# Optimization experiments

Hardware: AMD Instinct MI355X
Metric: run time of the kernel (lower is better)

The kernel has to match this reference:

```python
import jax, jax.numpy as jnp
import numpy as np

B, T, D, H = 16, 2048, 1024, 1024  # batch, seq (effective block_size), n_embed, head_size


def setup_inputs() -> dict:
    key = jax.random.key(0)
    k1, k2, k3, k4 = jax.random.split(key, 4)
    x = jax.random.normal(k1, (B, T, D), dtype=jnp.float32)
    # torch Linear weight is [out,in]; store as [in,out] for x @ W
    s = 1.0 / np.sqrt(D)
    Wq = jax.random.uniform(k2, (D, H), dtype=jnp.float32, minval=-s, maxval=s)
    Wk = jax.random.uniform(k3, (D, H), dtype=jnp.float32, minval=-s, maxval=s)
    Wv = jax.random.uniform(k4, (D, H), dtype=jnp.float32, minval=-s, maxval=s)
    return {"x": x, "Wq": Wq, "Wk": Wk, "Wv": Wv}


def reference(x, Wq, Wk, Wv):
    # Single-head causal self-attention, NO 1/sqrt(d) scaling (faithful to source).
    q = x @ Wq  # [B,T,H]
    k = x @ Wk  # [B,T,H]
    v = x @ Wv  # [B,T,H]
    w = jnp.einsum('bth,bsh->bts', q, k)  # [B,T,T]
    Tn = x.shape[1]
    causal = jnp.tril(jnp.ones((Tn, Tn), dtype=bool))
    w = jnp.where(causal, w, -jnp.inf)
    w = jax.nn.softmax(w, axis=-1)
    # dropout is identity in eval mode
    out = jnp.einsum('bts,bsh->bth', w, v)  # [B,T,H]
    return out
```

## Files before the change

### kernel.cpp

```cpp
#include <hip/hip_runtime.h>
#include <hip/hip_bf16.h>


typedef _Float16 half8 __attribute__((ext_vector_type(8)));
typedef _Float16 half4v __attribute__((ext_vector_type(4)));
typedef float floatx4 __attribute__((ext_vector_type(4)));

#define TB 16
#define TT 2048
#define TD 1024

__global__ void cvt_f32_f16(const float* __restrict__ in, _Float16* __restrict__ out, long n) {
    long i = ((long)blockIdx.x * blockDim.x + threadIdx.x) * 4;
    long stride = (long)gridDim.x * blockDim.x * 4;
    for (; i < n; i += stride) {
        float4 f = *(const float4*)(in + i);
        half4v h;
        h[0] = (_Float16)f.x; h[1] = (_Float16)f.y;
        h[2] = (_Float16)f.z; h[3] = (_Float16)f.w;
        *(half4v*)(out + i) = h;
    }
}

__global__ void transpose_cvt_w(const float* __restrict__ in, _Float16* __restrict__ out) {
    __shared__ float tile[32][33];
    const int bx = blockIdx.x * 32, by = blockIdx.y * 32;
    const int tx = threadIdx.x, ty = threadIdx.y;
#pragma unroll
    for (int i = ty; i < 32; i += 8) tile[i][tx] = in[(long)(by + i) * 1024 + bx + tx];
    __syncthreads();
#pragma unroll
    for (int i = ty; i < 32; i += 8) out[(long)(bx + i) * 1024 + by + tx] = (_Float16)tile[tx][i];
}

__device__ __forceinline__ void gload16(const _Float16* g, _Float16* l) {
    __builtin_amdgcn_global_load_lds((const __attribute__((address_space(1))) void*)g,
                                     (__attribute__((address_space(3))) void*)l, 16, 0, 0);
}

template <int MODE>
__global__ __launch_bounds__(512, 2) void gemm256(const _Float16* __restrict__ A,
                                                  const _Float16* __restrict__ B,
                                                  void* __restrict__ Cout,
                                                  int K, int lda, int ldb, int ldc,
                                                  long sAb, long sBb, long sCb,
                                                  int tilesN, int tilesM) {
    __shared__ _Float16 lds[65536];
    const int tid = threadIdx.x, lane = tid & 63, w = tid >> 6;
    const int wr = w >> 2, wc = w & 3;

    int bx = blockIdx.x;
    {
        const int nwg = gridDim.x, q = nwg >> 3, r = nwg & 7;
        const int xcd = bx & 7, idx = bx >> 3;
        bx = (xcd < r ? xcd * (q + 1) : r * (q + 1) + (xcd - r) * q) + idx;
    }
    int ti, tj;
    if (MODE == 1) {
        int rd = bx; ti = 0;
        while (rd > ti) { rd -= ti + 1; ++ti; }
        tj = rd;
    } else {
        ti = bx / tilesN; tj = bx % tilesN;
        if (MODE == 2) ti = tilesM - 1 - ti;
    }
    const int b = blockIdx.y;
    A += (long)b * sAb;
    B += (long)b * sBb;
    const long m0 = (long)ti * 256, n0 = (long)tj * 256;
    const int nkt = (MODE == 2) ? (ti + 1) * 4 : (K >> 6);

    const int row0 = tid >> 2;
    const int co   = (((tid & 3) ^ ((tid >> 3) & 3)) << 3);
    const int fcol = ((((lane >> 4) ^ (lane >> 1)) & 3) << 3);
    const int arow = wr * 128 + (lane & 15);
    const int brow = wc * 64 + (lane & 15);

    auto Abase = [&](int buf, int kk) { return lds + ((buf * 2 + kk) << 13); };
    auto Bbase = [&](int buf, int kk) { return lds + 32768 + ((buf * 2 + kk) << 13); };

    auto stageA = [&](int buf, int kk, int kt) {
        const long kb = (long)kt * 64 + kk * 32 + co;
        _Float16* d = Abase(buf, kk) + (w << 9);
        gload16(A + (m0 + row0) * (long)lda + kb, d);
        gload16(A + (m0 + row0 + 128) * (long)lda + kb, d + 4096);
    };
    auto stageB = [&](int buf, int kk, int kt) {
        const long kb = (long)kt * 64 + kk * 32 + co;
        _Float16* d = Bbase(buf, kk) + (w << 9);
        gload16(B + (n0 + row0) * (long)ldb + kb, d);
        gload16(B + (n0 + row0 + 128) * (long)ldb + kb, d + 4096);
    };
    auto ldA = [&](int buf, int kk, int m) {
        return *(const half8*)(Abase(buf, kk) + (arow + m * 16) * 32 + fcol);
    };
    auto ldB = [&](int buf, int kk, int n) {
        return *(const half8*)(Bbase(buf, kk) + (brow + n * 16) * 32 + fcol);
    };

    floatx4 acc[8][4] = {};

#define MFMA16(MH)                                                                     \
    _Pragma("unroll") for (int mm = 0; mm < 4; ++mm)                                   \
    _Pragma("unroll") for (int nn = 0; nn < 4; ++nn)                                   \
        acc[(MH)*4 + mm][nn] =                                                         \
            __builtin_amdgcn_mfma_f32_16x16x32_f16(afr[mm], bfr[nn], acc[(MH)*4 + mm][nn], 0, 0, 0);

    stageA(0, 0, 0); stageB(0, 0, 0); stageA(0, 1, 0); stageB(0, 1, 0);
    asm volatile("s_waitcnt vmcnt(4)" ::: "memory");
    __builtin_amdgcn_s_barrier();

    for (int t = 0; t < nkt; ++t) {
        const int cur = t & 1, nxt = cur ^ 1;
        const bool pf = (t + 1 < nkt);
        const int kn = t + 1;
        half8 afr[4], bfr[4];
#pragma unroll
        for (int nn = 0; nn < 4; ++nn) bfr[nn] = ldB(cur, 0, nn);
#pragma unroll
        for (int mm = 0; mm < 4; ++mm) afr[mm] = ldA(cur, 0, mm);
        if (pf) stageA(nxt, 0, kn);
        __builtin_amdgcn_s_barrier();
        asm volatile("s_waitcnt lgkmcnt(0)" ::: "memory");
        __builtin_amdgcn_sched_barrier(0);
        __builtin_amdgcn_s_setprio(1);
        MFMA16(0)
        __builtin_amdgcn_s_setprio(0);
        __builtin_amdgcn_s_barrier();
#pragma unroll
        for (int mm = 0; mm < 4; ++mm) afr[mm] = ldA(cur, 0, mm + 4);
        if (pf) stageB(nxt, 0, kn);
        __builtin_amdgcn_s_barrier();
        asm volatile("s_waitcnt lgkmcnt(0)" ::: "memory");
        __builtin_amdgcn_sched_barrier(0);
        __builtin_amdgcn_s_setprio(1);
        MFMA16(1)
        __builtin_amdgcn_s_setprio(0);
        if (pf) { asm volatile("s_waitcnt vmcnt(4)" ::: "memory"); }
        else    { asm volatile("s_waitcnt vmcnt(0)" ::: "memory"); }
        __builtin_amdgcn_s_barrier();
#pragma unroll
        for (int nn = 0; nn < 4; ++nn) bfr[nn] = ldB(cur, 1, nn);
#pragma unroll
        for (int mm = 0; mm < 4; ++mm) afr[mm] = ldA(cur, 1, mm);
        if (pf) stageA(nxt, 1, kn);
        __builtin_amdgcn_s_barrier();
        asm volatile("s_waitcnt lgkmcnt(0)" ::: "memory");
        __builtin_amdgcn_sched_barrier(0);
        __builtin_amdgcn_s_setprio(1);
        MFMA16(0)
        __builtin_amdgcn_s_setprio(0);
        __builtin_amdgcn_s_barrier();
#pragma unroll
        for (int mm = 0; mm < 4; ++mm) afr[mm] = ldA(cur, 1, mm + 4);
        if (pf) stageB(nxt, 1, kn);
        __builtin_amdgcn_s_barrier();
        asm volatile("s_waitcnt lgkmcnt(0)" ::: "memory");
        __builtin_amdgcn_sched_barrier(0);
        __builtin_amdgcn_s_setprio(1);
        MFMA16(1)
        __builtin_amdgcn_s_setprio(0);
        asm volatile("s_waitcnt vmcnt(4)" ::: "memory");
        __builtin_amdgcn_s_barrier();
    }
#undef MFMA16

    const int r4 = (lane >> 4) * 4, ccol = lane & 15;
    if (MODE <= 1) {
        _Float16* C = (_Float16*)Cout + (long)b * sCb;
#pragma unroll
        for (int m = 0; m < 8; ++m) {
            const long rbase = m0 + wr * 128 + m * 16 + r4;
#pragma unroll
            for (int n = 0; n < 4; ++n) {
                const long cbase = n0 + wc * 64 + n * 16 + ccol;
#pragma unroll
                for (int j = 0; j < 4; ++j)
                    C[(rbase + j) * (long)ldc + cbase] = (_Float16)acc[m][n][j];
            }
        }
    } else {
        float* C = (float*)Cout + (long)b * sCb;
#pragma unroll
        for (int m = 0; m < 8; ++m) {
            const long rbase = m0 + wr * 128 + m * 16 + r4;
#pragma unroll
            for (int n = 0; n < 4; ++n) {
                const long cbase = n0 + wc * 64 + n * 16 + ccol;
#pragma unroll
                for (int j = 0; j < 4; ++j)
                    C[(rbase + j) * (long)ldc + cbase] = acc[m][n][j];
            }
        }
    }
}

__device__ __forceinline__ float blockReduce(float v, bool ismax, float* sb) {
#pragma unroll
    for (int o = 32; o; o >>= 1) {
        float t = __shfl_xor(v, o);
        v = ismax ? fmaxf(v, t) : v + t;
    }
    if ((threadIdx.x & 63) == 0) sb[threadIdx.x >> 6] = v;
    __syncthreads();
    v = ismax ? fmaxf(fmaxf(sb[0], sb[1]), fmaxf(sb[2], sb[3]))
              : (sb[0] + sb[1]) + (sb[2] + sb[3]);
    __syncthreads();
    return v;
}

__global__ __launch_bounds__(256) void softmax_rows_f16(_Float16* __restrict__ S, int T) {
    __shared__ float sb[4];
    const long row = blockIdx.x;
    const int t = (int)(row % T);
    _Float16* s = S + row * (long)T;
    const int tid = threadIdx.x;
    const bool ld = (tid * 8 <= t);
    const int nstore = ((t >> 8) + 1) << 5;

    float v[8];
    float mx = -__builtin_inff();
    if (ld) {
        half8 hv = *(const half8*)(s + tid * 8);
#pragma unroll
        for (int j = 0; j < 8; ++j) {
            v[j] = (tid * 8 + j <= t) ? (float)hv[j] : -__builtin_inff();
            mx = fmaxf(mx, v[j]);
        }
    } else {
#pragma unroll
        for (int j = 0; j < 8; ++j) v[j] = -__builtin_inff();
    }
    const float m = blockReduce(mx, true, sb);

    float sum = 0.f;
#pragma unroll
    for (int j = 0; j < 8; ++j) {
        float p = __expf(v[j] - m);
        v[j] = p;
        sum += p;
    }
    const float l = blockReduce(sum, false, sb);
    const float inv = 1.f / l;

    if (tid < nstore) {
        half8 o;
#pragma unroll
        for (int j = 0; j < 8; ++j) o[j] = (_Float16)(v[j] * inv);
        *(half8*)(s + tid * 8) = o;
    }
}

extern "C" void kernel_launch(void* const* d_in, const int* in_sizes, int n_in,
                              void* d_out, int out_size, void* d_ws, size_t ws_size,
                              hipStream_t stream) {
    const float* x  = (const float*)d_in[0];
    const float* Wq = (const float*)d_in[1];
    const float* Wk = (const float*)d_in[2];
    const float* Wv = (const float*)d_in[3];
    float* out = (float*)d_out;

    const size_t XB = (size_t)TB * TT * TD;

    _Float16* x16 = (_Float16*)d_out;
    _Float16* Kh  = (_Float16*)d_out + XB;

    char* ws = (char*)d_ws;
    size_t off = 0;
    auto carve = [&](size_t bytes) { char* p = ws + off; off = (off + bytes + 255) & ~(size_t)255; return p; };
    _Float16* wqt = (_Float16*)carve((size_t)TD * TD * 2);
    _Float16* wkt = (_Float16*)carve((size_t)TD * TD * 2);
    _Float16* wvt = (_Float16*)carve((size_t)TD * TD * 2);
    _Float16* Qh  = (_Float16*)carve(XB * 2);
    _Float16* Vt  = (_Float16*)carve(XB * 2);

    const size_t CH = (size_t)TT * TT * 2;
    int NB = 16;
    while (NB > 1 && off + (size_t)NB * CH > ws_size) NB >>= 1;
    _Float16* Sc = (_Float16*)carve((size_t)NB * CH);

    cvt_f32_f16<<<2048, 256, 0, stream>>>(x, x16, (long)XB);
    transpose_cvt_w<<<dim3(32, 32), dim3(32, 8), 0, stream>>>(Wq, wqt);
    transpose_cvt_w<<<dim3(32, 32), dim3(32, 8), 0, stream>>>(Wk, wkt);
    transpose_cvt_w<<<dim3(32, 32), dim3(32, 8), 0, stream>>>(Wv, wvt);

    gemm256<0><<<dim3(128 * 4, 1), 512, 0, stream>>>(x16, wqt, Qh, TD, TD, TD, TD,
                                                     0, 0, 0, 4, 128);
    gemm256<0><<<dim3(128 * 4, 1), 512, 0, stream>>>(x16, wkt, Kh, TD, TD, TD, TD,
                                                     0, 0, 0, 4, 128);
    gemm256<0><<<dim3(4 * 8, TB), 512, 0, stream>>>(wvt, x16, Vt, TD, TD, TD, TT,
                                                    0, (long)TT * TD, (long)TD * TT, 8, 4);

    for (int cb = 0; cb < TB; cb += NB) {
        gemm256<1><<<dim3(36, NB), 512, 0, stream>>>(Qh + (size_t)cb * TT * TD,
                                                     Kh + (size_t)cb * TT * TD, Sc,
                                                     TD, TD, TD, TT,
                                                     (long)TT * TD, (long)TT * TD, (long)TT * TT, 8, 8);
        softmax_rows_f16<<<NB * TT, 256, 0, stream>>>(Sc, TT);
        gemm256<2><<<dim3(8 * 4, NB), 512, 0, stream>>>(Sc, Vt + (size_t)cb * TD * TT,
                                                        out + (size_t)cb * TT * TD, TT,
                                                        TT, TT, TD,
                                                        (long)TT * TT, (long)TD * TT, (long)TT * TD, 4, 8);
    }
}
```

Baseline: 543.6 us.

## Fuse Q/K projections, reorder PV tiles by work, use warp-per-row softmax

Q and K projections now run as one GEMM launch with a doubled N dimension, and the epilogue routes the upper half of the tiles to the K buffer. The causal PV GEMM flattens batch into the x grid so that tiles with the heaviest K loops across all batches go first, with XCD remapping applied inside each row-group. Softmax now gives each row to one 64-lane wavefront, with four rows per block, so only shuffle reductions are needed and the LDS/syncthreads reductions go away. The aim is fewer launches, better load balance in the triangular PV stage, and less sync overhead in softmax, at the cost of more complex block-index mapping.

```diff
diff --git a/kernel.cpp b/kernel.cpp
--- a/kernel.cpp
+++ b/kernel.cpp
@@ -42,29 +42,36 @@
 __global__ __launch_bounds__(512, 2) void gemm256(const _Float16* __restrict__ A,
                                                   const _Float16* __restrict__ B,
                                                   void* __restrict__ Cout,
+                                                  void* __restrict__ Cout2,
                                                   int K, int lda, int ldb, int ldc,
                                                   long sAb, long sBb, long sCb,
-                                                  int tilesN, int tilesM) {
+                                                  int tilesN, int tilesM, int nb) {
     __shared__ _Float16 lds[65536];
     const int tid = threadIdx.x, lane = tid & 63, w = tid >> 6;
     const int wr = w >> 2, wc = w & 3;
 
-    int bx = blockIdx.x;
-    {
-        const int nwg = gridDim.x, q = nwg >> 3, r = nwg & 7;
-        const int xcd = bx & 7, idx = bx >> 3;
+    int b, ti, tj;
+    if (MODE == 2) {
+        const int grp = nb * 4;
+        const int g = blockIdx.x / grp;
+        ti = tilesM - 1 - g;
+        int i2 = blockIdx.x - g * grp;
+        const int q = grp >> 3, r = grp & 7, xcd = i2 & 7, idx = i2 >> 3;
+        i2 = (xcd < r ? xcd * (q + 1) : r * (q + 1) + (xcd - r) * q) + idx;
+        b = i2 >> 2; tj = i2 & 3;
+    } else {
+        int bx = blockIdx.x;
+        const int nwg = gridDim.x, q = nwg >> 3, r = nwg & 7, xcd = bx & 7, idx = bx >> 3;
         bx = (xcd < r ? xcd * (q + 1) : r * (q + 1) + (xcd - r) * q) + idx;
-    }
-    int ti, tj;
-    if (MODE == 1) {
-        int rd = bx; ti = 0;
-        while (rd > ti) { rd -= ti + 1; ++ti; }
-        tj = rd;
-    } else {
-        ti = bx / tilesN; tj = bx % tilesN;
-        if (MODE == 2) ti = tilesM - 1 - ti;
-    }
-    const int b = blockIdx.y;
+        b = blockIdx.y;
+        if (MODE == 1) {
+            int rd = bx; ti = 0;
+            while (rd > ti) { rd -= ti + 1; ++ti; }
+            tj = rd;
+        } else {
+            ti = bx / tilesN; tj = bx % tilesN;
+        }
+    }
     A += (long)b * sAb;
     B += (long)b * sBb;
     const long m0 = (long)ti * 256, n0 = (long)tj * 256;
@@ -166,14 +173,17 @@
 #undef MFMA16
 
     const int r4 = (lane >> 4) * 4, ccol = lane & 15;
-    if (MODE <= 1) {
-        _Float16* C = (_Float16*)Cout + (long)b * sCb;
+    if (MODE != 2) {
+        _Float16* C;
+        long nb0 = n0;
+        if (MODE == 3 && n0 >= TD) { C = (_Float16*)Cout2; nb0 = n0 - TD; }
+        else                        C = (_Float16*)Cout + (long)b * sCb;
 #pragma unroll
         for (int m = 0; m < 8; ++m) {
             const long rbase = m0 + wr * 128 + m * 16 + r4;
 #pragma unroll
             for (int n = 0; n < 4; ++n) {
-                const long cbase = n0 + wc * 64 + n * 16 + ccol;
+                const long cbase = nb0 + wc * 64 + n * 16 + ccol;
 #pragma unroll
                 for (int j = 0; j < 4; ++j)
                     C[(rbase + j) * (long)ldc + cbase] = (_Float16)acc[m][n][j];
@@ -195,59 +205,55 @@
     }
 }
 
-__device__ __forceinline__ float blockReduce(float v, bool ismax, float* sb) {
-#pragma unroll
-    for (int o = 32; o; o >>= 1) {
-        float t = __shfl_xor(v, o);
-        v = ismax ? fmaxf(v, t) : v + t;
-    }
-    if ((threadIdx.x & 63) == 0) sb[threadIdx.x >> 6] = v;
-    __syncthreads();
-    v = ismax ? fmaxf(fmaxf(sb[0], sb[1]), fmaxf(sb[2], sb[3]))
-              : (sb[0] + sb[1]) + (sb[2] + sb[3]);
-    __syncthreads();
-    return v;
-}
-
 __global__ __launch_bounds__(256) void softmax_rows_f16(_Float16* __restrict__ S, int T) {
-    __shared__ float sb[4];
-    const long row = blockIdx.x;
-    const int t = (int)(row % T);
+    const int wv = threadIdx.x >> 6, lane = threadIdx.x & 63;
+    const long row = (long)blockIdx.x * 4 + wv;
+    const int t = (int)(row & (T - 1));
     _Float16* s = S + row * (long)T;
-    const int tid = threadIdx.x;
-    const bool ld = (tid * 8 <= t);
-    const int nstore = ((t >> 8) + 1) << 5;
-
-    float v[8];
+    const int nstore = ((t >> 8) + 1) << 8;
+
+    float v[4][8];
     float mx = -__builtin_inff();
-    if (ld) {
-        half8 hv = *(const half8*)(s + tid * 8);
+#pragma unroll
+    for (int c = 0; c < 4; ++c) {
+        const int col0 = (c * 64 + lane) * 8;
+        if (col0 <= t) {
+            half8 hv = *(const half8*)(s + col0);
+#pragma unroll
+            for (int j = 0; j < 8; ++j) {
+                v[c][j] = (col0 + j <= t) ? (float)hv[j] : -__builtin_inff();
+                mx = fmaxf(mx, v[c][j]);
+            }
+        } else {
+#pragma unroll
+            for (int j = 0; j < 8; ++j) v[c][j] = -__builtin_inff();
+        }
+    }
+#pragma unroll
+    for (int o = 32; o; o >>= 1) mx = fmaxf(mx, __shfl_xor(mx, o));
+
+    float sum = 0.f;
+#pragma unroll
+    for (int c = 0; c < 4; ++c)
 #pragma unroll
         for (int j = 0; j < 8; ++j) {
-            v[j] = (tid * 8 + j <= t) ? (float)hv[j] : -__builtin_inff();
-            mx = fmaxf(mx, v[j]);
-        }
-    } else {
-#pragma unroll
-        for (int j = 0; j < 8; ++j) v[j] = -__builtin_inff();
-    }
-    const float m = blockReduce(mx, true, sb);
-
-    float sum = 0.f;
-#pragma unroll
-    for (int j = 0; j < 8; ++j) {
-        float p = __expf(v[j] - m);
-        v[j] = p;
-        sum += p;
-    }
-    const float l = blockReduce(sum, false, sb);
-    const float inv = 1.f / l;
-
-    if (tid < nstore) {
-        half8 o;
-#pragma unroll
-        for (int j = 0; j < 8; ++j) o[j] = (_Float16)(v[j] * inv);
-        *(half8*)(s + tid * 8) = o;
+            float p = __expf(v[c][j] - mx);
+            v[c][j] = p;
+            sum += p;
+        }
+#pragma unroll
+    for (int o = 32; o; o >>= 1) sum += __shfl_xor(sum, o);
+    const float inv = 1.f / sum;
+
+#pragma unroll
+    for (int c = 0; c < 4; ++c) {
+        const int col0 = (c * 64 + lane) * 8;
+        if (col0 < nstore) {
+            half8 o;
+#pragma unroll
+            for (int j = 0; j < 8; ++j) o[j] = (_Float16)(v[c][j] * inv);
+            *(half8*)(s + col0) = o;
+        }
     }
 }
 
@@ -284,22 +290,20 @@
     transpose_cvt_w<<<dim3(32, 32), dim3(32, 8), 0, stream>>>(Wk, wkt);
     transpose_cvt_w<<<dim3(32, 32), dim3(32, 8), 0, stream>>>(Wv, wvt);
 
-    gemm256<0><<<dim3(128 * 4, 1), 512, 0, stream>>>(x16, wqt, Qh, TD, TD, TD, TD,
-                                                     0, 0, 0, 4, 128);
-    gemm256<0><<<dim3(128 * 4, 1), 512, 0, stream>>>(x16, wkt, Kh, TD, TD, TD, TD,
-                                                     0, 0, 0, 4, 128);
-    gemm256<0><<<dim3(4 * 8, TB), 512, 0, stream>>>(wvt, x16, Vt, TD, TD, TD, TT,
-                                                    0, (long)TT * TD, (long)TD * TT, 8, 4);
+    gemm256<3><<<dim3(128 * 8, 1), 512, 0, stream>>>(x16, wqt, Qh, Kh, TD, TD, TD, TD,
+                                                     0, 0, 0, 8, 128, 0);
+    gemm256<0><<<dim3(4 * 8, TB), 512, 0, stream>>>(wvt, x16, Vt, nullptr, TD, TD, TD, TT,
+                                                    0, (long)TT * TD, (long)TD * TT, 8, 4, 0);
 
     for (int cb = 0; cb < TB; cb += NB) {
         gemm256<1><<<dim3(36, NB), 512, 0, stream>>>(Qh + (size_t)cb * TT * TD,
-                                                     Kh + (size_t)cb * TT * TD, Sc,
+                                                     Kh + (size_t)cb * TT * TD, Sc, nullptr,
                                                      TD, TD, TD, TT,
-                                                     (long)TT * TD, (long)TT * TD, (long)TT * TT, 8, 8);
-        softmax_rows_f16<<<NB * TT, 256, 0, stream>>>(Sc, TT);
-        gemm256<2><<<dim3(8 * 4, NB), 512, 0, stream>>>(Sc, Vt + (size_t)cb * TD * TT,
-                                                        out + (size_t)cb * TT * TD, TT,
-                                                        TT, TT, TD,
-                                                        (long)TT * TT, (long)TD * TT, (long)TT * TD, 4, 8);
-    }
-}
+                                                     (long)TT * TD, (long)TT * TD, (long)TT * TT, 8, 8, 0);
+        softmax_rows_f16<<<NB * TT / 4, 256, 0, stream>>>(Sc, TT);
+        gemm256<2><<<dim3(NB * 32, 1), 512, 0, stream>>>(Sc, Vt + (size_t)cb * TD * TT,
+                                                         out + (size_t)cb * TT * TD, nullptr, TT,
+                                                         TT, TT, TD,
+                                                         (long)TT * TT, (long)TD * TT, (long)TT * TD, 4, 8, NB);
+    }
+}
```

After: 483.5 us. 1.12x faster.
